# Kernel optimization log

Measured on AMD Instinct MI355X. Metric: run time of the kernel, lower is better.

## Reference

```python
import jax, jax.numpy as jnp
import numpy as np

EPS = 1e-5

def layernorm2d(x, w, b):
    # nn.LayerNorm([T, C]): normalize jointly over last two dims, affine shape [T, C]
    mu = jnp.mean(x, axis=(-2, -1), keepdims=True)
    var = jnp.mean(jnp.square(x - mu), axis=(-2, -1), keepdims=True)
    return (x - mu) * jax.lax.rsqrt(var + EPS) * w + b


def setup_inputs() -> dict:
    key = jax.random.key(0)
    ks = jax.random.split(key, 10)
    B, T, C = 64, 512, 512
    s = 0.02
    inputs = jax.random.normal(ks[0], (B, T, C), dtype=jnp.float32)
    ln1_w = jnp.ones((T, C), dtype=jnp.float32)
    ln1_b = jnp.zeros((T, C), dtype=jnp.float32)
    ln2_w = jnp.ones((T, C), dtype=jnp.float32)
    ln2_b = jnp.zeros((T, C), dtype=jnp.float32)
    # TriU: row i holds the Linear(i+1,1) weights for prefix 0..i -> lower-triangular [T,T]
    tri_M = jax.random.normal(ks[1], (T, T), dtype=jnp.float32) * s
    tri_b = jax.random.normal(ks[2], (T,), dtype=jnp.float32) * s
    d1_w = jax.random.normal(ks[3], (C, C), dtype=jnp.float32) * s  # dense_1: out = x @ d1_w.T + d1_b
    d1_b = jax.random.normal(ks[4], (C,), dtype=jnp.float32) * s
    d2_w = jax.random.normal(ks[5], (C, C), dtype=jnp.float32) * s
    d2_b = jax.random.normal(ks[6], (C,), dtype=jnp.float32) * s
    return {"inputs": inputs, "ln1_w": ln1_w, "ln1_b": ln1_b,
            "ln2_w": ln2_w, "ln2_b": ln2_b,
            "tri_M": tri_M, "tri_b": tri_b,
            "d1_w": d1_w, "d1_b": d1_b, "d2_w": d2_w, "d2_b": d2_b}


def reference(inputs, ln1_w, ln1_b, ln2_w, ln2_b, tri_M, tri_b, d1_w, d1_b, d2_w, d2_b):
    # x: [B, T, C]
    x = layernorm2d(inputs, ln1_w, ln1_b)
    # TriU time mixer: out[b,i,c] = sum_{j<=i} M[i,j] * x[b,j,c] + tri_b[i]
    M = jnp.tril(tri_M)
    x = jnp.einsum('it,btc->bic', M, x) + tri_b[None, :, None]
    x = layernorm2d(x + inputs, ln2_w, ln2_b)
    # channel mixer MLP (dropout = 0)
    h = jax.nn.gelu(jnp.einsum('btc,hc->bth', x, d1_w) + d1_b, approximate=False)
    y = jnp.einsum('bth,ch->btc', h, d2_w) + d2_b
    return x + y
```

## Files before the change

### kernel.cpp

```cpp
#include <hip/hip_runtime.h>
#include <hip/hip_bf16.h>
#include <math.h>


#define B_ 64
#define T_ 512
#define C_ 512
#define TC_ (T_ * C_)
static_assert(TC_ == 262144, "");

typedef __attribute__((ext_vector_type(8))) short bf16x8;
typedef __attribute__((ext_vector_type(4))) float f32x4;

__device__ __forceinline__ unsigned short f2bf(float f) {
  union { float f; unsigned u; } v; v.f = f;
  unsigned r = v.u + 0x7FFF + ((v.u >> 16) & 1);
  return (unsigned short)(r >> 16);
}
__device__ __forceinline__ float bf2f(unsigned short h) {
  union { unsigned u; float f; } v; v.u = ((unsigned)h) << 16; return v.f;
}

__device__ __forceinline__ void load16_lds(const void* gsrc, void* ldst) {
  __builtin_amdgcn_global_load_lds(
      (const __attribute__((address_space(1))) unsigned int*)gsrc,
      (__attribute__((address_space(3))) unsigned int*)ldst,
      16, 0, 0);
}

__global__ __launch_bounds__(256) void prep(
    const float* __restrict__ triM, const float* __restrict__ d1w,
    const float* __restrict__ d2w, unsigned short* __restrict__ Mb,
    unsigned short* __restrict__ W1b, unsigned short* __restrict__ W2b,
    const float* __restrict__ x, float* __restrict__ red) {
  if (blockIdx.x < 1024) {
    const int idx = blockIdx.x * 256 + threadIdx.x;
    const int i = idx >> 9, j = idx & 511;
    Mb[idx]  = (j <= i) ? f2bf(triM[idx]) : (unsigned short)0;
    W1b[idx] = f2bf(d1w[idx]);
    W2b[idx] = f2bf(d2w[idx]);
    return;
  }
  const int bb = blockIdx.x - 1024;
  const int b = bb >> 4;
  const int s = bb & 15;
  const float4* p = (const float4*)(x + (size_t)b * TC_) + (size_t)s * 4096;
  float s1 = 0.f, s2 = 0.f;
  for (int i = threadIdx.x; i < 4096; i += 256) {
    float4 v = p[i];
    s1 += v.x + v.y + v.z + v.w;
    s2 += v.x * v.x + v.y * v.y + v.z * v.z + v.w * v.w;
  }
#pragma unroll
  for (int o = 32; o; o >>= 1) { s1 += __shfl_down(s1, o, 64); s2 += __shfl_down(s2, o, 64); }
  __shared__ float sm[8];
  const int w = threadIdx.x >> 6, lane = threadIdx.x & 63;
  if (lane == 0) { sm[w * 2] = s1; sm[w * 2 + 1] = s2; }
  __syncthreads();
  if (threadIdx.x == 0) {
    float a = 0.f, c = 0.f;
    for (int i = 0; i < 4; ++i) { a += sm[2 * i]; c += sm[2 * i + 1]; }
    atomicAdd(&red[b * 2], a);
    atomicAdd(&red[b * 2 + 1], c);
  }
}

__global__ __launch_bounds__(256) void ln1_norm_t(
    const float* __restrict__ x, const float* __restrict__ w,
    const float* __restrict__ bvec, const float* __restrict__ red1,
    unsigned short* __restrict__ XnT) {
  __shared__ unsigned short tile[64][65];
  const int b = blockIdx.z;
  const int t0 = blockIdx.y * 64;
  const int c0 = blockIdx.x * 64;
  const float mu = red1[b * 2] * (1.f / TC_);
  const float rstd = rsqrtf(red1[b * 2 + 1] * (1.f / TC_) - mu * mu + 1e-5f);
  const int tid = threadIdx.x;
  const int r = tid >> 4;
  const int cg = (tid & 15) * 4;
#pragma unroll
  for (int rr = 0; rr < 4; ++rr) {
    const int t = t0 + rr * 16 + r;
    const float4 xv = *(const float4*)&x[((size_t)b * T_ + t) * C_ + c0 + cg];
    const float4 wv = *(const float4*)&w[(size_t)t * C_ + c0 + cg];
    const float4 bv = *(const float4*)&bvec[(size_t)t * C_ + c0 + cg];
    tile[rr * 16 + r][cg + 0] = f2bf((xv.x - mu) * rstd * wv.x + bv.x);
    tile[rr * 16 + r][cg + 1] = f2bf((xv.y - mu) * rstd * wv.y + bv.y);
    tile[rr * 16 + r][cg + 2] = f2bf((xv.z - mu) * rstd * wv.z + bv.z);
    tile[rr * 16 + r][cg + 3] = f2bf((xv.w - mu) * rstd * wv.w + bv.w);
  }
  __syncthreads();
  const int cl = tid >> 2;
  const int tg = (tid & 3) * 16;
  alignas(16) unsigned short tmp[16];
#pragma unroll
  for (int j = 0; j < 16; ++j) tmp[j] = tile[tg + j][cl];
  unsigned short* o = &XnT[((size_t)b * C_ + c0 + cl) * T_ + t0 + tg];
  *(uint4*)&o[0] = *(const uint4*)&tmp[0];
  *(uint4*)&o[8] = *(const uint4*)&tmp[8];
}

__device__ __forceinline__ void stage_tile128(
    const unsigned short* __restrict__ Ag, const unsigned short* __restrict__ Bg,
    int k0, unsigned short* As, unsigned short* Bs, int tid) {
  const int row = tid >> 2;
  const int l = ((tid & 3) ^ ((row >> 1) & 3)) * 8;
  load16_lds(Ag + ((size_t)row << 9) + k0 + l, As + tid * 8);
  load16_lds(Bg + ((size_t)row << 9) + k0 + l, Bs + tid * 8);
}

__device__ __forceinline__ void mfma_tile128(
    const unsigned short* __restrict__ As, const unsigned short* __restrict__ Bs,
    int arow, int brow, int co, f32x4 acc[4][2]) {
  bf16x8 af[4], bfr[2];
#pragma unroll
  for (int m = 0; m < 4; ++m)
    af[m] = *(const bf16x8*)&As[arow + m * 512 + co];
#pragma unroll
  for (int n = 0; n < 2; ++n)
    bfr[n] = *(const bf16x8*)&Bs[brow + n * 512 + co];
  __builtin_amdgcn_s_setprio(1);
#pragma unroll
  for (int m = 0; m < 4; ++m)
#pragma unroll
    for (int n = 0; n < 2; ++n)
      acc[m][n] = __builtin_amdgcn_mfma_f32_16x16x32_bf16(af[m], bfr[n], acc[m][n], 0, 0, 0);
  __builtin_amdgcn_s_setprio(0);
}

__device__ __forceinline__ void gemm_mainloop128(
    const unsigned short* __restrict__ Ag, const unsigned short* __restrict__ Bg,
    int ktiles,
    unsigned short* lds, f32x4 acc[4][2], int tid) {
  const int lane = tid & 63;
  const int w = tid >> 6;
  const int wm = w >> 2, wn = w & 3;
  const int m16 = lane & 15, quad = lane >> 4;
  unsigned short* A0 = lds;
  unsigned short* B0 = lds + 4096;
  unsigned short* A1 = lds + 8192;
  unsigned short* B1 = lds + 12288;
  const int arow = (wm * 64 + m16) * 32;
  const int brow = (wn * 32 + m16) * 32;
  const int co = (quad ^ ((m16 >> 1) & 3)) * 8;
  stage_tile128(Ag, Bg, 0, A0, B0, tid);
  __syncthreads();
  for (int kt = 0; kt < ktiles; kt += 2) {
    stage_tile128(Ag, Bg, (kt + 1) * 32, A1, B1, tid);
    mfma_tile128(A0, B0, arow, brow, co, acc);
    __syncthreads();
    if (kt + 2 < ktiles)
      stage_tile128(Ag, Bg, (kt + 2) * 32, A0, B0, tid);
    mfma_tile128(A1, B1, arow, brow, co, acc);
    __syncthreads();
  }
}

__device__ __forceinline__ int xcd_swizzle_1024(int bid) {
  return ((bid & 7) << 7) | (bid >> 3);
}

__global__ __launch_bounds__(512, 4) void gemm_mixer(
    const unsigned short* __restrict__ Mb, const unsigned short* __restrict__ XnT,
    const float* __restrict__ trib, const float* __restrict__ inp,
    unsigned short* __restrict__ Z, float* __restrict__ red2) {
  __shared__ __align__(16) unsigned short lds[16384];
  const int swz = xcd_swizzle_1024((int)blockIdx.x);
  const int b = swz >> 4;
  const int i0 = ((swz >> 2) & 3) * 128;
  const int c0 = (swz & 3) * 128;
  f32x4 acc[4][2];
#pragma unroll
  for (int m = 0; m < 4; ++m)
#pragma unroll
    for (int n = 0; n < 2; ++n) acc[m][n] = (f32x4){0.f, 0.f, 0.f, 0.f};
  gemm_mainloop128(Mb + (size_t)i0 * T_, XnT + (size_t)b * TC_ + (size_t)c0 * T_,
                   (i0 >> 5) + 4, lds, acc, (int)threadIdx.x);
  const int tid = threadIdx.x, lane = tid & 63, w = tid >> 6;
  const int wm = w >> 2, wn = w & 3, m16 = lane & 15, quad = lane >> 4;
  const int rbase = i0 + wm * 64, cbase = c0 + wn * 32;
  float s1 = 0.f, s2 = 0.f;
#pragma unroll
  for (int m = 0; m < 4; ++m) {
#pragma unroll
    for (int g = 0; g < 4; ++g) {
      const int i = rbase + m * 16 + quad * 4 + g;
      const float tb = trib[i];
      const float* inrow = &inp[((size_t)b * T_ + i) * C_];
      unsigned short* zrow = &Z[((size_t)b * T_ + i) * C_];
#pragma unroll
      for (int n = 0; n < 2; ++n) {
        const int ch = cbase + n * 16 + m16;
        const float v = acc[m][n][g] + tb + inrow[ch];
        zrow[ch] = f2bf(v);
        s1 += v; s2 += v * v;
      }
    }
  }
#pragma unroll
  for (int o = 32; o; o >>= 1) { s1 += __shfl_down(s1, o, 64); s2 += __shfl_down(s2, o, 64); }
  __shared__ float smf[16];
  if (lane == 0) { smf[w * 2] = s1; smf[w * 2 + 1] = s2; }
  __syncthreads();
  if (tid == 0) {
    float a = 0.f, c2 = 0.f;
    for (int i = 0; i < 8; ++i) { a += smf[2 * i]; c2 += smf[2 * i + 1]; }
    atomicAdd(&red2[b * 2], a);
    atomicAdd(&red2[b * 2 + 1], c2);
  }
}

__global__ __launch_bounds__(256) void ln2_norm(
    const unsigned short* __restrict__ Z, const float* __restrict__ red2,
    const float* __restrict__ w, const float* __restrict__ bvec,
    unsigned short* __restrict__ X2) {
  const size_t e = ((size_t)blockIdx.x * 256 + threadIdx.x) * 8;
  const int b = (int)(e >> 18);
  const int tc = (int)(e & (TC_ - 1));
  const float mu = red2[b * 2] * (1.f / TC_);
  const float rstd = rsqrtf(red2[b * 2 + 1] * (1.f / TC_) - mu * mu + 1e-5f);
  uint4 zp = *(const uint4*)&Z[e];
  const unsigned short* zs = (const unsigned short*)&zp;
  alignas(16) float wv[8], bb[8];
  *(float4*)&wv[0] = *(const float4*)&w[tc];
  *(float4*)&wv[4] = *(const float4*)&w[tc + 4];
  *(float4*)&bb[0] = *(const float4*)&bvec[tc];
  *(float4*)&bb[4] = *(const float4*)&bvec[tc + 4];
  alignas(16) unsigned short o[8];
#pragma unroll
  for (int j = 0; j < 8; ++j)
    o[j] = f2bf((bf2f(zs[j]) - mu) * rstd * wv[j] + bb[j]);
  *(uint4*)&X2[e] = *(const uint4*)&o[0];
}

__global__ __launch_bounds__(512, 4) void gemm_d1(
    const unsigned short* __restrict__ X2, const unsigned short* __restrict__ W1b,
    const float* __restrict__ d1b, unsigned short* __restrict__ H) {
  __shared__ __align__(16) unsigned short lds[16384];
  const int swz = xcd_swizzle_1024((int)blockIdx.x);
  const int i0 = (swz & 255) * 128;
  const int n0 = (swz >> 8) * 128;
  f32x4 acc[4][2];
#pragma unroll
  for (int m = 0; m < 4; ++m)
#pragma unroll
    for (int n = 0; n < 2; ++n) acc[m][n] = (f32x4){0.f, 0.f, 0.f, 0.f};
  gemm_mainloop128(X2 + (size_t)i0 * C_, W1b + (size_t)n0 * C_, 16, lds, acc,
                   (int)threadIdx.x);
  const int tid = threadIdx.x, lane = tid & 63, w = tid >> 6;
  const int wm = w >> 2, wn = w & 3, m16 = lane & 15, quad = lane >> 4;
  const int rbase = i0 + wm * 64, cbase = n0 + wn * 32;
#pragma unroll
  for (int m = 0; m < 4; ++m) {
#pragma unroll
    for (int g = 0; g < 4; ++g) {
      const int row = rbase + m * 16 + quad * 4 + g;
#pragma unroll
      for (int n = 0; n < 2; ++n) {
        const int col = cbase + n * 16 + m16;
        const float v = acc[m][n][g] + d1b[col];
        const float gl = 0.5f * v * (1.0f + erff(v * 0.70710678118654752f));
        H[(size_t)row * C_ + col] = f2bf(gl);
      }
    }
  }
}

__global__ __launch_bounds__(512, 4) void gemm_d2(
    const unsigned short* __restrict__ H, const unsigned short* __restrict__ W2b,
    const float* __restrict__ d2b, const unsigned short* __restrict__ X2,
    float* __restrict__ out) {
  __shared__ __align__(16) unsigned short lds[16384];
  const int swz = xcd_swizzle_1024((int)blockIdx.x);
  const int i0 = (swz & 255) * 128;
  const int n0 = (swz >> 8) * 128;
  f32x4 acc[4][2];
#pragma unroll
  for (int m = 0; m < 4; ++m)
#pragma unroll
    for (int n = 0; n < 2; ++n) acc[m][n] = (f32x4){0.f, 0.f, 0.f, 0.f};
  gemm_mainloop128(H + (size_t)i0 * C_, W2b + (size_t)n0 * C_, 16, lds, acc,
                   (int)threadIdx.x);
  const int tid = threadIdx.x, lane = tid & 63, w = tid >> 6;
  const int wm = w >> 2, wn = w & 3, m16 = lane & 15, quad = lane >> 4;
  const int rbase = i0 + wm * 64, cbase = n0 + wn * 32;
#pragma unroll
  for (int m = 0; m < 4; ++m) {
#pragma unroll
    for (int g = 0; g < 4; ++g) {
      const int row = rbase + m * 16 + quad * 4 + g;
#pragma unroll
      for (int n = 0; n < 2; ++n) {
        const int col = cbase + n * 16 + m16;
        out[(size_t)row * C_ + col] =
            acc[m][n][g] + d2b[col] + bf2f(X2[(size_t)row * C_ + col]);
      }
    }
  }
}

extern "C" void kernel_launch(void* const* d_in, const int* in_sizes, int n_in,
                              void* d_out, int out_size, void* d_ws, size_t ws_size,
                              hipStream_t stream) {
  const float* inp  = (const float*)d_in[0];
  const float* ln1w = (const float*)d_in[1];
  const float* ln1b = (const float*)d_in[2];
  const float* ln2w = (const float*)d_in[3];
  const float* ln2b = (const float*)d_in[4];
  const float* triM = (const float*)d_in[5];
  const float* trib = (const float*)d_in[6];
  const float* d1w  = (const float*)d_in[7];
  const float* d1b  = (const float*)d_in[8];
  const float* d2w  = (const float*)d_in[9];
  const float* d2b  = (const float*)d_in[10];
  float* out = (float*)d_out;

  char* ws = (char*)d_ws;
  float* red1 = (float*)ws;
  float* red2 = (float*)(ws + 512);
  unsigned short* Mb  = (unsigned short*)(ws + 1024);
  unsigned short* W1b = Mb + TC_;
  unsigned short* W2b = W1b + TC_;
  unsigned short* XnT = W2b + TC_;
  unsigned short* Z   = XnT + (size_t)B_ * TC_;
  unsigned short* X2  = Z + (size_t)B_ * TC_;
  unsigned short* H   = X2 + (size_t)B_ * TC_;

  hipMemsetAsync(ws, 0, 1024, stream);
  prep<<<2048, 256, 0, stream>>>(triM, d1w, d2w, Mb, W1b, W2b, inp, red1);
  ln1_norm_t<<<dim3(8, 8, B_), 256, 0, stream>>>(inp, ln1w, ln1b, red1, XnT);
  gemm_mixer<<<1024, 512, 0, stream>>>(Mb, XnT, trib, inp, Z, red2);
  ln2_norm<<<8192, 256, 0, stream>>>(Z, red2, ln2w, ln2b, X2);
  gemm_d1<<<1024, 512, 0, stream>>>(X2, W1b, d1b, H);
  gemm_d2<<<1024, 512, 0, stream>>>(H, W2b, d2b, X2, out);
}
```

Baseline: 261.1 us.

## Fuse LN2, dense_1+GELU and dense_2 into one MLP kernel with LDS-resident activations

Replaces the separate ln2_norm, gemm_d1 and gemm_d2 kernels with one kernel. Each block normalizes a 32-row slab of Z into LDS, computes the full 512-wide hidden layer with GELU into LDS, then runs the second GEMM and adds the residual read from LDS. This removes the global round trips for X2 and H and two launches. In exchange the weight B-operands are read directly from global memory every k-step with no LDS staging or double buffering, and the 32-row tiles give less weight reuse, so the GEMMs may become bound on weight fetch latency or L2 bandwidth.

```diff
diff --git a/kernel.cpp b/kernel.cpp
--- a/kernel.cpp
+++ b/kernel.cpp
@@ -130,8 +130,7 @@
 
 __device__ __forceinline__ void gemm_mainloop128(
     const unsigned short* __restrict__ Ag, const unsigned short* __restrict__ Bg,
-    int ktiles,
-    unsigned short* lds, f32x4 acc[4][2], int tid) {
+    int ktiles, unsigned short* lds, f32x4 acc[4][2], int tid) {
   const int lane = tid & 63;
   const int w = tid >> 6;
   const int wm = w >> 2, wn = w & 3;
@@ -210,90 +209,117 @@
   }
 }
 
-__global__ __launch_bounds__(256) void ln2_norm(
+__global__ __launch_bounds__(512, 4) void gemm_mlp(
     const unsigned short* __restrict__ Z, const float* __restrict__ red2,
-    const float* __restrict__ w, const float* __restrict__ bvec,
-    unsigned short* __restrict__ X2) {
-  const size_t e = ((size_t)blockIdx.x * 256 + threadIdx.x) * 8;
-  const int b = (int)(e >> 18);
-  const int tc = (int)(e & (TC_ - 1));
+    const float* __restrict__ ln2w, const float* __restrict__ ln2b,
+    const unsigned short* __restrict__ W1b, const float* __restrict__ d1b,
+    const unsigned short* __restrict__ W2b, const float* __restrict__ d2b,
+    float* __restrict__ out) {
+  __shared__ __align__(16) unsigned short A1[32 * 512];
+  __shared__ __align__(16) unsigned short Hs[32 * 512];
+  const int bid = (int)blockIdx.x;
+  const int b = bid >> 4;
+  const int t0 = (bid & 15) * 32;
+  const int tid = threadIdx.x;
   const float mu = red2[b * 2] * (1.f / TC_);
   const float rstd = rsqrtf(red2[b * 2 + 1] * (1.f / TC_) - mu * mu + 1e-5f);
-  uint4 zp = *(const uint4*)&Z[e];
-  const unsigned short* zs = (const unsigned short*)&zp;
-  alignas(16) float wv[8], bb[8];
-  *(float4*)&wv[0] = *(const float4*)&w[tc];
-  *(float4*)&wv[4] = *(const float4*)&w[tc + 4];
-  *(float4*)&bb[0] = *(const float4*)&bvec[tc];
-  *(float4*)&bb[4] = *(const float4*)&bvec[tc + 4];
-  alignas(16) unsigned short o[8];
-#pragma unroll
-  for (int j = 0; j < 8; ++j)
-    o[j] = f2bf((bf2f(zs[j]) - mu) * rstd * wv[j] + bb[j]);
-  *(uint4*)&X2[e] = *(const uint4*)&o[0];
-}
-
-__global__ __launch_bounds__(512, 4) void gemm_d1(
-    const unsigned short* __restrict__ X2, const unsigned short* __restrict__ W1b,
-    const float* __restrict__ d1b, unsigned short* __restrict__ H) {
-  __shared__ __align__(16) unsigned short lds[16384];
-  const int swz = xcd_swizzle_1024((int)blockIdx.x);
-  const int i0 = (swz & 255) * 128;
-  const int n0 = (swz >> 8) * 128;
-  f32x4 acc[4][2];
-#pragma unroll
-  for (int m = 0; m < 4; ++m)
-#pragma unroll
-    for (int n = 0; n < 2; ++n) acc[m][n] = (f32x4){0.f, 0.f, 0.f, 0.f};
-  gemm_mainloop128(X2 + (size_t)i0 * C_, W1b + (size_t)n0 * C_, 16, lds, acc,
-                   (int)threadIdx.x);
-  const int tid = threadIdx.x, lane = tid & 63, w = tid >> 6;
-  const int wm = w >> 2, wn = w & 3, m16 = lane & 15, quad = lane >> 4;
-  const int rbase = i0 + wm * 64, cbase = n0 + wn * 32;
-#pragma unroll
-  for (int m = 0; m < 4; ++m) {
-#pragma unroll
-    for (int g = 0; g < 4; ++g) {
-      const int row = rbase + m * 16 + quad * 4 + g;
-#pragma unroll
-      for (int n = 0; n < 2; ++n) {
+
+#pragma unroll
+  for (int j = 0; j < 4; ++j) {
+    const int c = tid + 512 * j;
+    const int row = c >> 6;
+    const int cin = c & 63;
+    const int col = cin * 8;
+    const size_t g = ((size_t)b * T_ + t0 + row) * C_ + col;
+    uint4 zp = *(const uint4*)&Z[g];
+    const unsigned short* zs = (const unsigned short*)&zp;
+    const float* wrow = &ln2w[(size_t)(t0 + row) * C_ + col];
+    const float* brow = &ln2b[(size_t)(t0 + row) * C_ + col];
+    alignas(16) unsigned short o8[8];
+#pragma unroll
+    for (int e = 0; e < 8; ++e)
+      o8[e] = f2bf((bf2f(zs[e]) - mu) * rstd * wrow[e] + brow[e]);
+    *(uint4*)&A1[row * 512 + ((cin ^ (row & 7)) * 8)] = *(const uint4*)&o8[0];
+  }
+  __syncthreads();
+
+  const int lane = tid & 63, w = tid >> 6;
+  const int m16 = lane & 15, quad = lane >> 4;
+  const int cbase = w * 64;
+  const int key = m16 & 7;
+
+  f32x4 acc[2][4];
+#pragma unroll
+  for (int m = 0; m < 2; ++m)
+#pragma unroll
+    for (int n = 0; n < 4; ++n) acc[m][n] = (f32x4){0.f, 0.f, 0.f, 0.f};
+#pragma unroll 4
+  for (int kt = 0; kt < 16; ++kt) {
+    const int kq = kt * 4 + quad;
+    bf16x8 af[2], bfr[4];
+    af[0] = *(const bf16x8*)&A1[m16 * 512 + ((kq ^ key) * 8)];
+    af[1] = *(const bf16x8*)&A1[(16 + m16) * 512 + ((kq ^ key) * 8)];
+#pragma unroll
+    for (int n = 0; n < 4; ++n)
+      bfr[n] = *(const bf16x8*)&W1b[(size_t)(cbase + n * 16 + m16) * C_ + kq * 8];
+    __builtin_amdgcn_s_setprio(1);
+#pragma unroll
+    for (int m = 0; m < 2; ++m)
+#pragma unroll
+      for (int n = 0; n < 4; ++n)
+        acc[m][n] = __builtin_amdgcn_mfma_f32_16x16x32_bf16(af[m], bfr[n], acc[m][n], 0, 0, 0);
+    __builtin_amdgcn_s_setprio(0);
+  }
+#pragma unroll
+  for (int m = 0; m < 2; ++m) {
+#pragma unroll
+    for (int n = 0; n < 4; ++n) {
+#pragma unroll
+      for (int g = 0; g < 4; ++g) {
+        const int row = m * 16 + quad * 4 + g;
         const int col = cbase + n * 16 + m16;
         const float v = acc[m][n][g] + d1b[col];
         const float gl = 0.5f * v * (1.0f + erff(v * 0.70710678118654752f));
-        H[(size_t)row * C_ + col] = f2bf(gl);
+        Hs[row * 512 + (((col >> 3) ^ (row & 7)) * 8) + (col & 7)] = f2bf(gl);
       }
     }
   }
-}
-
-__global__ __launch_bounds__(512, 4) void gemm_d2(
-    const unsigned short* __restrict__ H, const unsigned short* __restrict__ W2b,
-    const float* __restrict__ d2b, const unsigned short* __restrict__ X2,
-    float* __restrict__ out) {
-  __shared__ __align__(16) unsigned short lds[16384];
-  const int swz = xcd_swizzle_1024((int)blockIdx.x);
-  const int i0 = (swz & 255) * 128;
-  const int n0 = (swz >> 8) * 128;
-  f32x4 acc[4][2];
-#pragma unroll
-  for (int m = 0; m < 4; ++m)
-#pragma unroll
-    for (int n = 0; n < 2; ++n) acc[m][n] = (f32x4){0.f, 0.f, 0.f, 0.f};
-  gemm_mainloop128(H + (size_t)i0 * C_, W2b + (size_t)n0 * C_, 16, lds, acc,
-                   (int)threadIdx.x);
-  const int tid = threadIdx.x, lane = tid & 63, w = tid >> 6;
-  const int wm = w >> 2, wn = w & 3, m16 = lane & 15, quad = lane >> 4;
-  const int rbase = i0 + wm * 64, cbase = n0 + wn * 32;
-#pragma unroll
-  for (int m = 0; m < 4; ++m) {
-#pragma unroll
-    for (int g = 0; g < 4; ++g) {
-      const int row = rbase + m * 16 + quad * 4 + g;
-#pragma unroll
-      for (int n = 0; n < 2; ++n) {
+  __syncthreads();
+
+  f32x4 acc2[2][4];
+#pragma unroll
+  for (int m = 0; m < 2; ++m)
+#pragma unroll
+    for (int n = 0; n < 4; ++n) acc2[m][n] = (f32x4){0.f, 0.f, 0.f, 0.f};
+#pragma unroll 4
+  for (int kt = 0; kt < 16; ++kt) {
+    const int kq = kt * 4 + quad;
+    bf16x8 af[2], bfr[4];
+    af[0] = *(const bf16x8*)&Hs[m16 * 512 + ((kq ^ key) * 8)];
+    af[1] = *(const bf16x8*)&Hs[(16 + m16) * 512 + ((kq ^ key) * 8)];
+#pragma unroll
+    for (int n = 0; n < 4; ++n)
+      bfr[n] = *(const bf16x8*)&W2b[(size_t)(cbase + n * 16 + m16) * C_ + kq * 8];
+    __builtin_amdgcn_s_setprio(1);
+#pragma unroll
+    for (int m = 0; m < 2; ++m)
+#pragma unroll
+      for (int n = 0; n < 4; ++n)
+        acc2[m][n] = __builtin_amdgcn_mfma_f32_16x16x32_bf16(af[m], bfr[n], acc2[m][n], 0, 0, 0);
+    __builtin_amdgcn_s_setprio(0);
+  }
+#pragma unroll
+  for (int m = 0; m < 2; ++m) {
+#pragma unroll
+    for (int n = 0; n < 4; ++n) {
+#pragma unroll
+      for (int g = 0; g < 4; ++g) {
+        const int row = m * 16 + quad * 4 + g;
         const int col = cbase + n * 16 + m16;
-        out[(size_t)row * C_ + col] =
-            acc[m][n][g] + d2b[col] + bf2f(X2[(size_t)row * C_ + col]);
+        const float resid =
+            bf2f(A1[row * 512 + (((col >> 3) ^ (row & 7)) * 8) + (col & 7)]);
+        out[((size_t)b * T_ + t0 + row) * C_ + col] =
+            acc2[m][n][g] + d2b[col] + resid;
       }
     }
   }
@@ -323,14 +349,10 @@
   unsigned short* W2b = W1b + TC_;
   unsigned short* XnT = W2b + TC_;
   unsigned short* Z   = XnT + (size_t)B_ * TC_;
-  unsigned short* X2  = Z + (size_t)B_ * TC_;
-  unsigned short* H   = X2 + (size_t)B_ * TC_;
 
   hipMemsetAsync(ws, 0, 1024, stream);
   prep<<<2048, 256, 0, stream>>>(triM, d1w, d2w, Mb, W1b, W2b, inp, red1);
   ln1_norm_t<<<dim3(8, 8, B_), 256, 0, stream>>>(inp, ln1w, ln1b, red1, XnT);
   gemm_mixer<<<1024, 512, 0, stream>>>(Mb, XnT, trib, inp, Z, red2);
-  ln2_norm<<<8192, 256, 0, stream>>>(Z, red2, ln2w, ln2b, X2);
-  gemm_d1<<<1024, 512, 0, stream>>>(X2, W1b, d1b, H);
-  gemm_d2<<<1024, 512, 0, stream>>>(H, W2b, d2b, X2, out);
-}
+  gemm_mlp<<<1024, 512, 0, stream>>>(Z, red2, ln2w, ln2b, W1b, d1b, W2b, d2b, out);
+}
```

Result: slower. 306.6 us (+17.4%).

## Fuse LN2 normalization into d1 GEMM A-staging and d2 epilogue residual

Applied to the files above, without the earlier changes.

Removes the standalone ln2_norm kernel and the X2 buffer. The normalized Z is now computed on the fly while staging A tiles in gemm_d1, and again in the gemm_d2 epilogue to rebuild the residual. LN2 weights and biases are pre-converted to bf16 in prep. The LN1 atomics and memset are replaced by per-slice partial sums that ln1_norm_t reduces itself. This saves a full read-write pass over the activation tensor and one launch, but d1 A loads become register loads with ALU work instead of direct-to-LDS loads, and the ln2 affine terms get rounded to bf16.

```diff
diff --git a/kernel.cpp b/kernel.cpp
--- a/kernel.cpp
+++ b/kernel.cpp
@@ -30,20 +30,25 @@
 
 __global__ __launch_bounds__(256) void prep(
     const float* __restrict__ triM, const float* __restrict__ d1w,
-    const float* __restrict__ d2w, unsigned short* __restrict__ Mb,
+    const float* __restrict__ d2w, const float* __restrict__ ln2w,
+    const float* __restrict__ ln2b, unsigned short* __restrict__ Mb,
     unsigned short* __restrict__ W1b, unsigned short* __restrict__ W2b,
-    const float* __restrict__ x, float* __restrict__ red) {
+    unsigned short* __restrict__ Lw, unsigned short* __restrict__ Lb,
+    const float* __restrict__ x, float* __restrict__ red1p,
+    float* __restrict__ red2) {
   if (blockIdx.x < 1024) {
+    if (blockIdx.x == 0 && threadIdx.x < 128) red2[threadIdx.x] = 0.f;
     const int idx = blockIdx.x * 256 + threadIdx.x;
     const int i = idx >> 9, j = idx & 511;
     Mb[idx]  = (j <= i) ? f2bf(triM[idx]) : (unsigned short)0;
     W1b[idx] = f2bf(d1w[idx]);
     W2b[idx] = f2bf(d2w[idx]);
+    Lw[idx]  = f2bf(ln2w[idx]);
+    Lb[idx]  = f2bf(ln2b[idx]);
     return;
   }
   const int bb = blockIdx.x - 1024;
-  const int b = bb >> 4;
-  const int s = bb & 15;
+  const int b = bb >> 4, s = bb & 15;
   const float4* p = (const float4*)(x + (size_t)b * TC_) + (size_t)s * 4096;
   float s1 = 0.f, s2 = 0.f;
   for (int i = threadIdx.x; i < 4096; i += 256) {
@@ -60,21 +65,27 @@
   if (threadIdx.x == 0) {
     float a = 0.f, c = 0.f;
     for (int i = 0; i < 4; ++i) { a += sm[2 * i]; c += sm[2 * i + 1]; }
-    atomicAdd(&red[b * 2], a);
-    atomicAdd(&red[b * 2 + 1], c);
+    red1p[bb * 2] = a;
+    red1p[bb * 2 + 1] = c;
   }
 }
 
 __global__ __launch_bounds__(256) void ln1_norm_t(
     const float* __restrict__ x, const float* __restrict__ w,
-    const float* __restrict__ bvec, const float* __restrict__ red1,
+    const float* __restrict__ bvec, const float* __restrict__ red1p,
     unsigned short* __restrict__ XnT) {
   __shared__ unsigned short tile[64][65];
   const int b = blockIdx.z;
   const int t0 = blockIdx.y * 64;
   const int c0 = blockIdx.x * 64;
-  const float mu = red1[b * 2] * (1.f / TC_);
-  const float rstd = rsqrtf(red1[b * 2 + 1] * (1.f / TC_) - mu * mu + 1e-5f);
+  float s1 = 0.f, s2 = 0.f;
+#pragma unroll
+  for (int i = 0; i < 16; ++i) {
+    s1 += red1p[(b * 16 + i) * 2];
+    s2 += red1p[(b * 16 + i) * 2 + 1];
+  }
+  const float mu = s1 * (1.f / TC_);
+  const float rstd = rsqrtf(s2 * (1.f / TC_) - mu * mu + 1e-5f);
   const int tid = threadIdx.x;
   const int r = tid >> 4;
   const int cg = (tid & 15) * 4;
@@ -109,6 +120,13 @@
   load16_lds(Bg + ((size_t)row << 9) + k0 + l, Bs + tid * 8);
 }
 
+__device__ __forceinline__ void stage_b128(
+    const unsigned short* __restrict__ Bg, int k0, unsigned short* Bs, int tid) {
+  const int row = tid >> 2;
+  const int l = ((tid & 3) ^ ((row >> 1) & 3)) * 8;
+  load16_lds(Bg + ((size_t)row << 9) + k0 + l, Bs + tid * 8);
+}
+
 __device__ __forceinline__ void mfma_tile128(
     const unsigned short* __restrict__ As, const unsigned short* __restrict__ Bs,
     int arow, int brow, int co, f32x4 acc[4][2]) {
@@ -130,8 +148,7 @@
 
 __device__ __forceinline__ void gemm_mainloop128(
     const unsigned short* __restrict__ Ag, const unsigned short* __restrict__ Bg,
-    int ktiles,
-    unsigned short* lds, f32x4 acc[4][2], int tid) {
+    int ktiles, unsigned short* lds, f32x4 acc[4][2], int tid) {
   const int lane = tid & 63;
   const int w = tid >> 6;
   const int wm = w >> 2, wn = w & 3;
@@ -210,45 +227,85 @@
   }
 }
 
-__global__ __launch_bounds__(256) void ln2_norm(
+__global__ __launch_bounds__(512, 4) void gemm_d1f(
     const unsigned short* __restrict__ Z, const float* __restrict__ red2,
-    const float* __restrict__ w, const float* __restrict__ bvec,
-    unsigned short* __restrict__ X2) {
-  const size_t e = ((size_t)blockIdx.x * 256 + threadIdx.x) * 8;
-  const int b = (int)(e >> 18);
-  const int tc = (int)(e & (TC_ - 1));
-  const float mu = red2[b * 2] * (1.f / TC_);
-  const float rstd = rsqrtf(red2[b * 2 + 1] * (1.f / TC_) - mu * mu + 1e-5f);
-  uint4 zp = *(const uint4*)&Z[e];
-  const unsigned short* zs = (const unsigned short*)&zp;
-  alignas(16) float wv[8], bb[8];
-  *(float4*)&wv[0] = *(const float4*)&w[tc];
-  *(float4*)&wv[4] = *(const float4*)&w[tc + 4];
-  *(float4*)&bb[0] = *(const float4*)&bvec[tc];
-  *(float4*)&bb[4] = *(const float4*)&bvec[tc + 4];
-  alignas(16) unsigned short o[8];
-#pragma unroll
-  for (int j = 0; j < 8; ++j)
-    o[j] = f2bf((bf2f(zs[j]) - mu) * rstd * wv[j] + bb[j]);
-  *(uint4*)&X2[e] = *(const uint4*)&o[0];
-}
-
-__global__ __launch_bounds__(512, 4) void gemm_d1(
-    const unsigned short* __restrict__ X2, const unsigned short* __restrict__ W1b,
-    const float* __restrict__ d1b, unsigned short* __restrict__ H) {
+    const unsigned short* __restrict__ Lw, const unsigned short* __restrict__ Lb,
+    const unsigned short* __restrict__ W1b, const float* __restrict__ d1b,
+    unsigned short* __restrict__ H) {
   __shared__ __align__(16) unsigned short lds[16384];
   const int swz = xcd_swizzle_1024((int)blockIdx.x);
   const int i0 = (swz & 255) * 128;
   const int n0 = (swz >> 8) * 128;
+  const int tid = (int)threadIdx.x;
+  const int batch = i0 >> 9;
+  const float mu = red2[batch * 2] * (1.f / TC_);
+  const float rstd = rsqrtf(red2[batch * 2 + 1] * (1.f / TC_) - mu * mu + 1e-5f);
+
+  const int srow = tid >> 2;
+  const int sl = ((tid & 3) ^ ((srow >> 1) & 3)) * 8;
+  const int t = (i0 + srow) & 511;
+  const unsigned short* zrow = Z + ((size_t)(i0 + srow) << 9);
+  const unsigned short* wrow = Lw + ((size_t)t << 9);
+  const unsigned short* brw  = Lb + ((size_t)t << 9);
+  const unsigned short* Bg = W1b + (size_t)n0 * C_;
+
+  unsigned short* A0 = lds;
+  unsigned short* B0 = lds + 4096;
+  unsigned short* A1 = lds + 8192;
+  unsigned short* B1 = lds + 12288;
+
   f32x4 acc[4][2];
 #pragma unroll
   for (int m = 0; m < 4; ++m)
 #pragma unroll
     for (int n = 0; n < 2; ++n) acc[m][n] = (f32x4){0.f, 0.f, 0.f, 0.f};
-  gemm_mainloop128(X2 + (size_t)i0 * C_, W1b + (size_t)n0 * C_, 16, lds, acc,
-                   (int)threadIdx.x);
-  const int tid = threadIdx.x, lane = tid & 63, w = tid >> 6;
-  const int wm = w >> 2, wn = w & 3, m16 = lane & 15, quad = lane >> 4;
+  const int lane = tid & 63, wv = tid >> 6;
+  const int wm = wv >> 2, wn = wv & 3, m16 = lane & 15, quad = lane >> 4;
+  const int arow = (wm * 64 + m16) * 32;
+  const int brow_l = (wn * 32 + m16) * 32;
+  const int co = (quad ^ ((m16 >> 1) & 3)) * 8;
+
+  uint4 zp, wp, bp;
+  zp = *(const uint4*)&zrow[sl];
+  wp = *(const uint4*)&wrow[sl];
+  bp = *(const uint4*)&brw[sl];
+  {
+    const unsigned short* zs = (const unsigned short*)&zp;
+    const unsigned short* ws = (const unsigned short*)&wp;
+    const unsigned short* bs = (const unsigned short*)&bp;
+    alignas(16) unsigned short o8[8];
+#pragma unroll
+    for (int e = 0; e < 8; ++e)
+      o8[e] = f2bf((bf2f(zs[e]) - mu) * rstd * bf2f(ws[e]) + bf2f(bs[e]));
+    *(uint4*)&A0[tid * 8] = *(const uint4*)&o8[0];
+  }
+  stage_b128(Bg, 0, B0, tid);
+  __syncthreads();
+  for (int kt = 0; kt < 16; ++kt) {
+    unsigned short* Ac = (kt & 1) ? A1 : A0;
+    unsigned short* Bc = (kt & 1) ? B1 : B0;
+    unsigned short* An = (kt & 1) ? A0 : A1;
+    unsigned short* Bn = (kt & 1) ? B0 : B1;
+    const int k1 = (kt + 1) * 32;
+    if (kt + 1 < 16) {
+      zp = *(const uint4*)&zrow[k1 + sl];
+      wp = *(const uint4*)&wrow[k1 + sl];
+      bp = *(const uint4*)&brw[k1 + sl];
+      stage_b128(Bg, k1, Bn, tid);
+    }
+    mfma_tile128(Ac, Bc, arow, brow_l, co, acc);
+    if (kt + 1 < 16) {
+      const unsigned short* zs = (const unsigned short*)&zp;
+      const unsigned short* ws = (const unsigned short*)&wp;
+      const unsigned short* bs = (const unsigned short*)&bp;
+      alignas(16) unsigned short o8[8];
+#pragma unroll
+      for (int e = 0; e < 8; ++e)
+        o8[e] = f2bf((bf2f(zs[e]) - mu) * rstd * bf2f(ws[e]) + bf2f(bs[e]));
+      *(uint4*)&An[tid * 8] = *(const uint4*)&o8[0];
+    }
+    __syncthreads();
+  }
   const int rbase = i0 + wm * 64, cbase = n0 + wn * 32;
 #pragma unroll
   for (int m = 0; m < 4; ++m) {
@@ -266,14 +323,18 @@
   }
 }
 
-__global__ __launch_bounds__(512, 4) void gemm_d2(
+__global__ __launch_bounds__(512, 4) void gemm_d2f(
     const unsigned short* __restrict__ H, const unsigned short* __restrict__ W2b,
-    const float* __restrict__ d2b, const unsigned short* __restrict__ X2,
-    float* __restrict__ out) {
+    const float* __restrict__ d2b, const unsigned short* __restrict__ Z,
+    const float* __restrict__ red2, const unsigned short* __restrict__ Lw,
+    const unsigned short* __restrict__ Lb, float* __restrict__ out) {
   __shared__ __align__(16) unsigned short lds[16384];
   const int swz = xcd_swizzle_1024((int)blockIdx.x);
   const int i0 = (swz & 255) * 128;
   const int n0 = (swz >> 8) * 128;
+  const int batch = i0 >> 9;
+  const float mu = red2[batch * 2] * (1.f / TC_);
+  const float rstd = rsqrtf(red2[batch * 2 + 1] * (1.f / TC_) - mu * mu + 1e-5f);
   f32x4 acc[4][2];
 #pragma unroll
   for (int m = 0; m < 4; ++m)
@@ -289,11 +350,15 @@
 #pragma unroll
     for (int g = 0; g < 4; ++g) {
       const int row = rbase + m * 16 + quad * 4 + g;
+      const int t = row & 511;
 #pragma unroll
       for (int n = 0; n < 2; ++n) {
         const int col = cbase + n * 16 + m16;
-        out[(size_t)row * C_ + col] =
-            acc[m][n][g] + d2b[col] + bf2f(X2[(size_t)row * C_ + col]);
+        const float resid =
+            (bf2f(Z[(size_t)row * C_ + col]) - mu) * rstd *
+                bf2f(Lw[(size_t)t * C_ + col]) +
+            bf2f(Lb[(size_t)t * C_ + col]);
+        out[(size_t)row * C_ + col] = acc[m][n][g] + d2b[col] + resid;
       }
     }
   }
@@ -316,21 +381,21 @@
   float* out = (float*)d_out;
 
   char* ws = (char*)d_ws;
-  float* red1 = (float*)ws;
-  float* red2 = (float*)(ws + 512);
-  unsigned short* Mb  = (unsigned short*)(ws + 1024);
+  float* red1p = (float*)ws;
+  float* red2  = (float*)(ws + 8192);
+  unsigned short* Mb  = (unsigned short*)(ws + 16384);
   unsigned short* W1b = Mb + TC_;
   unsigned short* W2b = W1b + TC_;
-  unsigned short* XnT = W2b + TC_;
+  unsigned short* Lw  = W2b + TC_;
+  unsigned short* Lb  = Lw + TC_;
+  unsigned short* XnT = Lb + TC_;
   unsigned short* Z   = XnT + (size_t)B_ * TC_;
-  unsigned short* X2  = Z + (size_t)B_ * TC_;
-  unsigned short* H   = X2 + (size_t)B_ * TC_;
-
-  hipMemsetAsync(ws, 0, 1024, stream);
-  prep<<<2048, 256, 0, stream>>>(triM, d1w, d2w, Mb, W1b, W2b, inp, red1);
-  ln1_norm_t<<<dim3(8, 8, B_), 256, 0, stream>>>(inp, ln1w, ln1b, red1, XnT);
+  unsigned short* H   = Z + (size_t)B_ * TC_;
+
+  prep<<<2048, 256, 0, stream>>>(triM, d1w, d2w, ln2w, ln2b, Mb, W1b, W2b,
+                                 Lw, Lb, inp, red1p, red2);
+  ln1_norm_t<<<dim3(8, 8, B_), 256, 0, stream>>>(inp, ln1w, ln1b, red1p, XnT);
   gemm_mixer<<<1024, 512, 0, stream>>>(Mb, XnT, trib, inp, Z, red2);
-  ln2_norm<<<8192, 256, 0, stream>>>(Z, red2, ln2w, ln2b, X2);
-  gemm_d1<<<1024, 512, 0, stream>>>(X2, W1b, d1b, H);
-  gemm_d2<<<1024, 512, 0, stream>>>(H, W2b, d2b, X2, out);
-}
+  gemm_d1f<<<1024, 512, 0, stream>>>(Z, red2, Lw, Lb, W1b, d1b, H);
+  gemm_d2f<<<1024, 512, 0, stream>>>(H, W2b, d2b, Z, red2, Lw, Lb, out);
+}
```

Result: no change. 265.3 us (+1.6%).

## Double GEMM K-tile depth to 64 and replace LN1 atomics with partial sums

Applied to the files above, without the earlier changes.

The shared GEMM mainloop now stages 64-wide K tiles (two 16-byte loads per thread per operand, XOR swizzle over 8 chunks) and runs two MFMA k-steps per tile. This halves the number of barrier-separated iterations in the mixer, d1 and d2 GEMMs, at the cost of doubling LDS per block to 64 KB, which may reduce occupancy. Separately, LN1 statistics are written as per-slice partials that ln1_norm_t sums itself, and red2 is zeroed inside prep. This removes the memset launch and the atomics.

```diff
diff --git a/kernel.cpp b/kernel.cpp
--- a/kernel.cpp
+++ b/kernel.cpp
@@ -32,8 +32,10 @@
     const float* __restrict__ triM, const float* __restrict__ d1w,
     const float* __restrict__ d2w, unsigned short* __restrict__ Mb,
     unsigned short* __restrict__ W1b, unsigned short* __restrict__ W2b,
-    const float* __restrict__ x, float* __restrict__ red) {
+    const float* __restrict__ x, float* __restrict__ red1p,
+    float* __restrict__ red2) {
   if (blockIdx.x < 1024) {
+    if (blockIdx.x == 0 && threadIdx.x < 128) red2[threadIdx.x] = 0.f;
     const int idx = blockIdx.x * 256 + threadIdx.x;
     const int i = idx >> 9, j = idx & 511;
     Mb[idx]  = (j <= i) ? f2bf(triM[idx]) : (unsigned short)0;
@@ -42,8 +44,7 @@
     return;
   }
   const int bb = blockIdx.x - 1024;
-  const int b = bb >> 4;
-  const int s = bb & 15;
+  const int b = bb >> 4, s = bb & 15;
   const float4* p = (const float4*)(x + (size_t)b * TC_) + (size_t)s * 4096;
   float s1 = 0.f, s2 = 0.f;
   for (int i = threadIdx.x; i < 4096; i += 256) {
@@ -60,21 +61,27 @@
   if (threadIdx.x == 0) {
     float a = 0.f, c = 0.f;
     for (int i = 0; i < 4; ++i) { a += sm[2 * i]; c += sm[2 * i + 1]; }
-    atomicAdd(&red[b * 2], a);
-    atomicAdd(&red[b * 2 + 1], c);
+    red1p[bb * 2] = a;
+    red1p[bb * 2 + 1] = c;
   }
 }
 
 __global__ __launch_bounds__(256) void ln1_norm_t(
     const float* __restrict__ x, const float* __restrict__ w,
-    const float* __restrict__ bvec, const float* __restrict__ red1,
+    const float* __restrict__ bvec, const float* __restrict__ red1p,
     unsigned short* __restrict__ XnT) {
   __shared__ unsigned short tile[64][65];
   const int b = blockIdx.z;
   const int t0 = blockIdx.y * 64;
   const int c0 = blockIdx.x * 64;
-  const float mu = red1[b * 2] * (1.f / TC_);
-  const float rstd = rsqrtf(red1[b * 2 + 1] * (1.f / TC_) - mu * mu + 1e-5f);
+  float s1 = 0.f, s2 = 0.f;
+#pragma unroll
+  for (int i = 0; i < 16; ++i) {
+    s1 += red1p[(b * 16 + i) * 2];
+    s2 += red1p[(b * 16 + i) * 2 + 1];
+  }
+  const float mu = s1 * (1.f / TC_);
+  const float rstd = rsqrtf(s2 * (1.f / TC_) - mu * mu + 1e-5f);
   const int tid = threadIdx.x;
   const int r = tid >> 4;
   const int cg = (tid & 15) * 4;
@@ -100,35 +107,43 @@
   *(uint4*)&o[8] = *(const uint4*)&tmp[8];
 }
 
-__device__ __forceinline__ void stage_tile128(
+__device__ __forceinline__ void stage_tile64(
     const unsigned short* __restrict__ Ag, const unsigned short* __restrict__ Bg,
     int k0, unsigned short* As, unsigned short* Bs, int tid) {
-  const int row = tid >> 2;
-  const int l = ((tid & 3) ^ ((row >> 1) & 3)) * 8;
-  load16_lds(Ag + ((size_t)row << 9) + k0 + l, As + tid * 8);
-  load16_lds(Bg + ((size_t)row << 9) + k0 + l, Bs + tid * 8);
-}
-
-__device__ __forceinline__ void mfma_tile128(
+#pragma unroll
+  for (int j = 0; j < 2; ++j) {
+    const int c = tid + 512 * j;
+    const int row = c >> 3;
+    const int l = ((c & 7) ^ (row & 7)) * 8;
+    load16_lds(Ag + ((size_t)row << 9) + k0 + l, As + c * 8);
+    load16_lds(Bg + ((size_t)row << 9) + k0 + l, Bs + c * 8);
+  }
+}
+
+__device__ __forceinline__ void mfma_tile64(
     const unsigned short* __restrict__ As, const unsigned short* __restrict__ Bs,
-    int arow, int brow, int co, f32x4 acc[4][2]) {
-  bf16x8 af[4], bfr[2];
-#pragma unroll
-  for (int m = 0; m < 4; ++m)
-    af[m] = *(const bf16x8*)&As[arow + m * 512 + co];
-#pragma unroll
-  for (int n = 0; n < 2; ++n)
-    bfr[n] = *(const bf16x8*)&Bs[brow + n * 512 + co];
-  __builtin_amdgcn_s_setprio(1);
-#pragma unroll
-  for (int m = 0; m < 4; ++m)
+    int arow, int brow, int quad, int xk, f32x4 acc[4][2]) {
+#pragma unroll
+  for (int ks = 0; ks < 2; ++ks) {
+    const int co = (((ks * 4 + quad) ^ xk) * 8);
+    bf16x8 af[4], bfr[2];
+#pragma unroll
+    for (int m = 0; m < 4; ++m)
+      af[m] = *(const bf16x8*)&As[arow + m * 1024 + co];
 #pragma unroll
     for (int n = 0; n < 2; ++n)
-      acc[m][n] = __builtin_amdgcn_mfma_f32_16x16x32_bf16(af[m], bfr[n], acc[m][n], 0, 0, 0);
-  __builtin_amdgcn_s_setprio(0);
-}
-
-__device__ __forceinline__ void gemm_mainloop128(
+      bfr[n] = *(const bf16x8*)&Bs[brow + n * 1024 + co];
+    __builtin_amdgcn_s_setprio(1);
+#pragma unroll
+    for (int m = 0; m < 4; ++m)
+#pragma unroll
+      for (int n = 0; n < 2; ++n)
+        acc[m][n] = __builtin_amdgcn_mfma_f32_16x16x32_bf16(af[m], bfr[n], acc[m][n], 0, 0, 0);
+    __builtin_amdgcn_s_setprio(0);
+  }
+}
+
+__device__ __forceinline__ void gemm_mainloop64(
     const unsigned short* __restrict__ Ag, const unsigned short* __restrict__ Bg,
     int ktiles,
     unsigned short* lds, f32x4 acc[4][2], int tid) {
@@ -137,21 +152,21 @@
   const int wm = w >> 2, wn = w & 3;
   const int m16 = lane & 15, quad = lane >> 4;
   unsigned short* A0 = lds;
-  unsigned short* B0 = lds + 4096;
-  unsigned short* A1 = lds + 8192;
-  unsigned short* B1 = lds + 12288;
-  const int arow = (wm * 64 + m16) * 32;
-  const int brow = (wn * 32 + m16) * 32;
-  const int co = (quad ^ ((m16 >> 1) & 3)) * 8;
-  stage_tile128(Ag, Bg, 0, A0, B0, tid);
+  unsigned short* B0 = lds + 8192;
+  unsigned short* A1 = lds + 16384;
+  unsigned short* B1 = lds + 24576;
+  const int arow = (wm * 64 + m16) * 64;
+  const int brow = (wn * 32 + m16) * 64;
+  const int xk = m16 & 7;
+  stage_tile64(Ag, Bg, 0, A0, B0, tid);
   __syncthreads();
   for (int kt = 0; kt < ktiles; kt += 2) {
-    stage_tile128(Ag, Bg, (kt + 1) * 32, A1, B1, tid);
-    mfma_tile128(A0, B0, arow, brow, co, acc);
+    stage_tile64(Ag, Bg, (kt + 1) * 64, A1, B1, tid);
+    mfma_tile64(A0, B0, arow, brow, quad, xk, acc);
     __syncthreads();
     if (kt + 2 < ktiles)
-      stage_tile128(Ag, Bg, (kt + 2) * 32, A0, B0, tid);
-    mfma_tile128(A1, B1, arow, brow, co, acc);
+      stage_tile64(Ag, Bg, (kt + 2) * 64, A0, B0, tid);
+    mfma_tile64(A1, B1, arow, brow, quad, xk, acc);
     __syncthreads();
   }
 }
@@ -164,7 +179,7 @@
     const unsigned short* __restrict__ Mb, const unsigned short* __restrict__ XnT,
     const float* __restrict__ trib, const float* __restrict__ inp,
     unsigned short* __restrict__ Z, float* __restrict__ red2) {
-  __shared__ __align__(16) unsigned short lds[16384];
+  __shared__ __align__(16) unsigned short lds[32768];
   const int swz = xcd_swizzle_1024((int)blockIdx.x);
   const int b = swz >> 4;
   const int i0 = ((swz >> 2) & 3) * 128;
@@ -174,8 +189,8 @@
   for (int m = 0; m < 4; ++m)
 #pragma unroll
     for (int n = 0; n < 2; ++n) acc[m][n] = (f32x4){0.f, 0.f, 0.f, 0.f};
-  gemm_mainloop128(Mb + (size_t)i0 * T_, XnT + (size_t)b * TC_ + (size_t)c0 * T_,
-                   (i0 >> 5) + 4, lds, acc, (int)threadIdx.x);
+  gemm_mainloop64(Mb + (size_t)i0 * T_, XnT + (size_t)b * TC_ + (size_t)c0 * T_,
+                  (i0 >> 6) + 2, lds, acc, (int)threadIdx.x);
   const int tid = threadIdx.x, lane = tid & 63, w = tid >> 6;
   const int wm = w >> 2, wn = w & 3, m16 = lane & 15, quad = lane >> 4;
   const int rbase = i0 + wm * 64, cbase = c0 + wn * 32;
@@ -236,7 +251,7 @@
 __global__ __launch_bounds__(512, 4) void gemm_d1(
     const unsigned short* __restrict__ X2, const unsigned short* __restrict__ W1b,
     const float* __restrict__ d1b, unsigned short* __restrict__ H) {
-  __shared__ __align__(16) unsigned short lds[16384];
+  __shared__ __align__(16) unsigned short lds[32768];
   const int swz = xcd_swizzle_1024((int)blockIdx.x);
   const int i0 = (swz & 255) * 128;
   const int n0 = (swz >> 8) * 128;
@@ -245,8 +260,8 @@
   for (int m = 0; m < 4; ++m)
 #pragma unroll
     for (int n = 0; n < 2; ++n) acc[m][n] = (f32x4){0.f, 0.f, 0.f, 0.f};
-  gemm_mainloop128(X2 + (size_t)i0 * C_, W1b + (size_t)n0 * C_, 16, lds, acc,
-                   (int)threadIdx.x);
+  gemm_mainloop64(X2 + (size_t)i0 * C_, W1b + (size_t)n0 * C_, 8, lds, acc,
+                  (int)threadIdx.x);
   const int tid = threadIdx.x, lane = tid & 63, w = tid >> 6;
   const int wm = w >> 2, wn = w & 3, m16 = lane & 15, quad = lane >> 4;
   const int rbase = i0 + wm * 64, cbase = n0 + wn * 32;
@@ -270,7 +285,7 @@
     const unsigned short* __restrict__ H, const unsigned short* __restrict__ W2b,
     const float* __restrict__ d2b, const unsigned short* __restrict__ X2,
     float* __restrict__ out) {
-  __shared__ __align__(16) unsigned short lds[16384];
+  __shared__ __align__(16) unsigned short lds[32768];
   const int swz = xcd_swizzle_1024((int)blockIdx.x);
   const int i0 = (swz & 255) * 128;
   const int n0 = (swz >> 8) * 128;
@@ -279,8 +294,8 @@
   for (int m = 0; m < 4; ++m)
 #pragma unroll
     for (int n = 0; n < 2; ++n) acc[m][n] = (f32x4){0.f, 0.f, 0.f, 0.f};
-  gemm_mainloop128(H + (size_t)i0 * C_, W2b + (size_t)n0 * C_, 16, lds, acc,
-                   (int)threadIdx.x);
+  gemm_mainloop64(H + (size_t)i0 * C_, W2b + (size_t)n0 * C_, 8, lds, acc,
+                  (int)threadIdx.x);
   const int tid = threadIdx.x, lane = tid & 63, w = tid >> 6;
   const int wm = w >> 2, wn = w & 3, m16 = lane & 15, quad = lane >> 4;
   const int rbase = i0 + wm * 64, cbase = n0 + wn * 32;
@@ -316,9 +331,9 @@
   float* out = (float*)d_out;
 
   char* ws = (char*)d_ws;
-  float* red1 = (float*)ws;
-  float* red2 = (float*)(ws + 512);
-  unsigned short* Mb  = (unsigned short*)(ws + 1024);
+  float* red1p = (float*)ws;
+  float* red2  = (float*)(ws + 8192);
+  unsigned short* Mb  = (unsigned short*)(ws + 16384);
   unsigned short* W1b = Mb + TC_;
   unsigned short* W2b = W1b + TC_;
   unsigned short* XnT = W2b + TC_;
@@ -326,9 +341,8 @@
   unsigned short* X2  = Z + (size_t)B_ * TC_;
   unsigned short* H   = X2 + (size_t)B_ * TC_;
 
-  hipMemsetAsync(ws, 0, 1024, stream);
-  prep<<<2048, 256, 0, stream>>>(triM, d1w, d2w, Mb, W1b, W2b, inp, red1);
-  ln1_norm_t<<<dim3(8, 8, B_), 256, 0, stream>>>(inp, ln1w, ln1b, red1, XnT);
+  prep<<<2048, 256, 0, stream>>>(triM, d1w, d2w, Mb, W1b, W2b, inp, red1p, red2);
+  ln1_norm_t<<<dim3(8, 8, B_), 256, 0, stream>>>(inp, ln1w, ln1b, red1p, XnT);
   gemm_mixer<<<1024, 512, 0, stream>>>(Mb, XnT, trib, inp, Z, red2);
   ln2_norm<<<8192, 256, 0, stream>>>(Z, red2, ln2w, ln2b, X2);
   gemm_d1<<<1024, 512, 0, stream>>>(X2, W1b, d1b, H);
```

After: 248.1 us. -5.0%, faster.
